# Kernel optimization log

Hardware: AMD Instinct MI355X
Metric: run time of the kernel (lower is better)

The kernel has to match this reference:

```python
import jax, jax.numpy as jnp
import numpy as np

D = 1024
M = 4096


def _linear_params(key, fan_in, fan_out):
    kw, kb = jax.random.split(key)
    bound = 1.0 / np.sqrt(fan_in)
    W = jax.random.uniform(kw, (fan_out, fan_in), jnp.float32, -bound, bound)
    b = jax.random.uniform(kb, (fan_out,), jnp.float32, -bound, bound)
    return W, b


def setup_inputs() -> dict:
    key = jax.random.key(0)
    ks = jax.random.split(key, 6)
    x = jax.random.normal(ks[0], (4, 2048, D), jnp.float32)
    Wq, bq = _linear_params(ks[1], D, D)
    Wk, bk = _linear_params(ks[2], D, D)
    Wv, bv = _linear_params(ks[3], D, D)
    Wo, bo = _linear_params(ks[4], D, D)
    Wf, bf = _linear_params(ks[5], D, M)
    return {"x": x, "Wq": Wq, "bq": bq, "Wk": Wk, "bk": bk,
            "Wv": Wv, "bv": bv, "Wo": Wo, "bo": bo, "Wf": Wf, "bf": bf}


def reference(x, Wq, bq, Wk, bk, Wv, bv, Wo, bo, Wf, bf):
    # projections (torch Linear: x @ W.T + b)
    Q = x @ Wq.T + bq  # [B,S,D]
    K = x @ Wk.T + bk
    V = x @ Wv.T + bv
    d_k = Q.shape[-1]
    scores = jnp.einsum('bqd,bkd->bqk', Q, K) / jnp.sqrt(jnp.float32(d_k))
    S = scores.shape[-1]
    causal = jnp.tril(jnp.ones((S, S), dtype=bool))  # [S,S]
    scores = jnp.where(causal, scores, -jnp.inf)
    probs = jax.nn.softmax(scores, axis=-1)
    attn = jnp.einsum('bqk,bkd->bqd', probs, V)
    out = attn @ Wo.T + bo
    # FFN: Linear(d->m) + GELU (torch default: exact erf GELU)
    ff = jax.nn.gelu(out @ Wf.T + bf, approximate=False)
    return ff
```

## Files before the change

kernel.cpp:

```cpp
#include <hip/hip_runtime.h>
#include <hip/hip_bf16.h>
#include <math.h>

using bf16 = __hip_bfloat16;
typedef __attribute__((ext_vector_type(8))) short bf16x8;
typedef __attribute__((ext_vector_type(4))) short bf16x4;
typedef __attribute__((ext_vector_type(4))) float f32x4;

#define GLOBAL_AS __attribute__((address_space(1)))
#define LDS_AS __attribute__((address_space(3)))

__device__ __forceinline__ float b2f(bf16 v) { return __bfloat162float(v); }
__device__ __forceinline__ bf16 f2b(float v) { return __float2bfloat16(v); }

__global__ __launch_bounds__(256) void k_conv(const float* __restrict__ src,
                                              bf16* __restrict__ dst, int n4) {
  int i = blockIdx.x * 256 + threadIdx.x;
  if (i >= n4) return;
  float4 v = ((const float4*)src)[i];
  bf16 t[4] = {f2b(v.x), f2b(v.y), f2b(v.z), f2b(v.w)};
  *(bf16x4*)(dst + 4 * (size_t)i) = *(bf16x4*)t;
}

__device__ __forceinline__ void stage_async(const bf16* __restrict__ g,
                                            int ldg, bf16* __restrict__ s) {
  int lane = threadIdx.x & 63;
  int wave = threadIdx.x >> 6;
  bf16* lds = s + wave * 1024;
  const bf16* g0 = g + (size_t)(wave * 32 + (lane >> 2)) * ldg + ((lane & 3) << 3);
  const bf16* g1 = g0 + (size_t)16 * ldg;
  __builtin_amdgcn_global_load_lds((GLOBAL_AS const unsigned*)g0,
                                   (LDS_AS unsigned*)lds, 16, 0, 0);
  __builtin_amdgcn_global_load_lds((GLOBAL_AS const unsigned*)g1,
                                   (LDS_AS unsigned*)(lds + 512), 16, 0, 0);
}

struct Acc { f32x4 a[4][4]; };

__device__ __forceinline__ void gemm_core(const bf16* __restrict__ A,
                                          const bf16* __restrict__ B,
                                          int K, int lda, int ldb, Acc& acc,
                                          bf16* sA, bf16* sB) {
  int lane = threadIdx.x & 63;
  int wave = threadIdx.x >> 6;
  int wm = wave & 1, wn = wave >> 1;
  int r = lane & 15;
  int ko = (lane >> 4) << 3;

  for (int k0 = 0; k0 < K; k0 += 32) {
    stage_async(A + k0, lda, sA);
    stage_async(B + k0, ldb, sB);
    __syncthreads();
    bf16x8 af[4], bfr[4];
#pragma unroll
    for (int t = 0; t < 4; ++t) {
      af[t]  = *(const bf16x8*)(sA + (wm * 64 + t * 16 + r) * 32 + ko);
      bfr[t] = *(const bf16x8*)(sB + (wn * 64 + t * 16 + r) * 32 + ko);
    }
#pragma unroll
    for (int tm = 0; tm < 4; ++tm)
#pragma unroll
      for (int tn = 0; tn < 4; ++tn)
        acc.a[tm][tn] = __builtin_amdgcn_mfma_f32_16x16x32_bf16(
            af[tm], bfr[tn], acc.a[tm][tn], 0, 0, 0);
    __syncthreads();
  }
}

template <typename TO, bool BIAS, bool GELU>
__device__ __forceinline__ void epilogue(const Acc& acc, TO* __restrict__ C,
                                         int ldc, const float* __restrict__ bias,
                                         float scale) {
  int lane = threadIdx.x & 63;
  int wave = threadIdx.x >> 6;
  int wm = wave & 1, wn = wave >> 1;
  int rbase = wm * 64 + ((lane >> 4) << 2);
  int cbase = wn * 64 + (lane & 15);
#pragma unroll
  for (int tm = 0; tm < 4; ++tm) {
#pragma unroll
    for (int tn = 0; tn < 4; ++tn) {
      int nn = cbase + tn * 16;
      float bv = BIAS ? bias[nn] : 0.0f;
#pragma unroll
      for (int rr = 0; rr < 4; ++rr) {
        int mm = rbase + tm * 16 + rr;
        float c = acc.a[tm][tn][rr] * scale + bv;
        if (GELU) c = 0.5f * c * (1.0f + erff(c * 0.70710678118f));
        if constexpr (__hip_internal::is_same<TO, bf16>::value)
          C[(size_t)mm * ldc + nn] = f2b(c);
        else
          C[(size_t)mm * ldc + nn] = c;
      }
    }
  }
}

__global__ __launch_bounds__(256) void k_qkv(
    const bf16* __restrict__ X, const bf16* __restrict__ Wq,
    const bf16* __restrict__ Wk, const bf16* __restrict__ Wv,
    const float* __restrict__ bq, const float* __restrict__ bk,
    const float* __restrict__ bv,
    bf16* __restrict__ Q, bf16* __restrict__ Ko, bf16* __restrict__ Vt) {
  __shared__ alignas(16) bf16 sA[4096];
  __shared__ alignas(16) bf16 sB[4096];
  const int K = 1024, N = 1024;
  int z = blockIdx.z;
  const bf16* W     = (z == 0) ? Wq : (z == 1) ? Wk : Wv;
  const float* bias = (z == 0) ? bq : (z == 1) ? bk : bv;
  const bf16* A = X + (size_t)blockIdx.x * 128 * K;
  const bf16* B = W + (size_t)blockIdx.y * 128 * K;
  Acc acc = {};
  gemm_core(A, B, K, K, K, acc, sA, sB);

  if (z < 2) {
    bf16* C = (z == 0 ? Q : Ko) +
              (size_t)blockIdx.x * 128 * N + blockIdx.y * 128;
    epilogue<bf16, true, false>(acc, C, N, bias + blockIdx.y * 128, 1.0f);
  } else {
    int lane = threadIdx.x & 63;
    int wave = threadIdx.x >> 6;
    int wm = wave & 1, wn = wave >> 1;
    int rbase = blockIdx.x * 128 + wm * 64 + ((lane >> 4) << 2);
    int cbase = blockIdx.y * 128 + wn * 64 + (lane & 15);
#pragma unroll
    for (int tm = 0; tm < 4; ++tm)
#pragma unroll
      for (int tn = 0; tn < 4; ++tn) {
        int n = cbase + tn * 16;
        float bvv = bias[n];
#pragma unroll
        for (int rr = 0; rr < 4; ++rr) {
          int m = rbase + tm * 16 + rr;
          int b = m >> 11, s = m & 2047;
          float c = acc.a[tm][tn][rr] + bvv;
          Vt[((size_t)b * 1024 + n) * 2048 + s] = f2b(c);
        }
      }
  }
}

__global__ __launch_bounds__(256) void k_scores(const bf16* __restrict__ Q,
                                                const bf16* __restrict__ Kk,
                                                bf16* __restrict__ P) {
  int bx = 15 - blockIdx.x;
  if ((int)blockIdx.y > bx) return;
  __shared__ alignas(16) bf16 sA[4096];
  __shared__ alignas(16) bf16 sB[4096];
  const int K = 1024, S = 2048;
  int z = blockIdx.z;
  const bf16* A = Q  + (size_t)z * S * K + (size_t)bx * 128 * K;
  const bf16* B = Kk + (size_t)z * S * K + (size_t)blockIdx.y * 128 * K;
  Acc acc = {};
  gemm_core(A, B, K, K, K, acc, sA, sB);
  bf16* C = P + (size_t)z * S * S + (size_t)bx * 128 * S + blockIdx.y * 128;
  epilogue<bf16, false, false>(acc, C, S, nullptr, 0.03125f);
}

__global__ __launch_bounds__(256) void k_softmax(bf16* __restrict__ P) {
  const int S = 2048;
  int q = blockIdx.x, z = blockIdx.y;
  bf16* row = P + ((size_t)z * S + q) * S;
  __shared__ float red[4];
  int tid = threadIdx.x;

  float mx = -1e30f;
  for (int k = tid; k <= q; k += 256) mx = fmaxf(mx, b2f(row[k]));
#pragma unroll
  for (int o = 32; o > 0; o >>= 1) mx = fmaxf(mx, __shfl_xor(mx, o));
  if ((tid & 63) == 0) red[tid >> 6] = mx;
  __syncthreads();
  mx = fmaxf(fmaxf(red[0], red[1]), fmaxf(red[2], red[3]));
  __syncthreads();

  float sum = 0.0f;
  for (int k = tid; k <= q; k += 256) sum += expf(b2f(row[k]) - mx);
#pragma unroll
  for (int o = 32; o > 0; o >>= 1) sum += __shfl_xor(sum, o);
  if ((tid & 63) == 0) red[tid >> 6] = sum;
  __syncthreads();
  sum = red[0] + red[1] + red[2] + red[3];
  float inv = 1.0f / sum;

  int kcap = ((q >> 7) + 1) << 7;
  for (int k = tid; k < kcap; k += 256) {
    float p = (k <= q) ? expf(b2f(row[k]) - mx) * inv : 0.0f;
    row[k] = f2b(p);
  }
}

__global__ __launch_bounds__(256) void k_attn(const bf16* __restrict__ P,
                                              const bf16* __restrict__ Vt,
                                              bf16* __restrict__ O) {
  __shared__ alignas(16) bf16 sA[4096];
  __shared__ alignas(16) bf16 sB[4096];
  const int S = 2048, D = 1024;
  int bx = 15 - (int)blockIdx.x;
  int z = blockIdx.z;
  int Keff = (bx + 1) * 128;
  const bf16* A = P  + (size_t)z * S * S + (size_t)bx * 128 * S;
  const bf16* B = Vt + (size_t)z * D * S + (size_t)blockIdx.y * 128 * S;
  Acc acc = {};
  gemm_core(A, B, Keff, S, S, acc, sA, sB);
  bf16* C = O + (size_t)z * S * D + (size_t)bx * 128 * D + blockIdx.y * 128;
  epilogue<bf16, false, false>(acc, C, D, nullptr, 1.0f);
}

__global__ __launch_bounds__(256) void k_out(const bf16* __restrict__ A0,
                                             const bf16* __restrict__ W,
                                             const float* __restrict__ bias,
                                             bf16* __restrict__ C0) {
  __shared__ alignas(16) bf16 sA[4096];
  __shared__ alignas(16) bf16 sB[4096];
  const int K = 1024, N = 1024;
  const bf16* A = A0 + (size_t)blockIdx.x * 128 * K;
  const bf16* B = W + (size_t)blockIdx.y * 128 * K;
  Acc acc = {};
  gemm_core(A, B, K, K, K, acc, sA, sB);
  bf16* C = C0 + (size_t)blockIdx.x * 128 * N + blockIdx.y * 128;
  epilogue<bf16, true, false>(acc, C, N, bias + blockIdx.y * 128, 1.0f);
}

__global__ __launch_bounds__(256) void k_ffn(const bf16* __restrict__ A0,
                                             const bf16* __restrict__ W,
                                             const float* __restrict__ bias,
                                             float* __restrict__ C0) {
  __shared__ alignas(16) bf16 sA[4096];
  __shared__ alignas(16) bf16 sB[4096];
  const int K = 1024, N = 4096;
  const bf16* A = A0 + (size_t)blockIdx.x * 128 * K;
  const bf16* B = W + (size_t)blockIdx.y * 128 * K;
  Acc acc = {};
  gemm_core(A, B, K, K, K, acc, sA, sB);
  float* C = C0 + (size_t)blockIdx.x * 128 * N + blockIdx.y * 128;
  epilogue<float, true, true>(acc, C, N, bias + blockIdx.y * 128, 1.0f);
}

extern "C" void kernel_launch(void* const* d_in, const int* in_sizes, int n_in,
                              void* d_out, int out_size, void* d_ws,
                              size_t ws_size, hipStream_t stream) {
  const float* x   = (const float*)d_in[0];
  const float* Wq  = (const float*)d_in[1];
  const float* bq  = (const float*)d_in[2];
  const float* Wk  = (const float*)d_in[3];
  const float* bk  = (const float*)d_in[4];
  const float* Wv  = (const float*)d_in[5];
  const float* bv  = (const float*)d_in[6];
  const float* Wo  = (const float*)d_in[7];
  const float* bo  = (const float*)d_in[8];
  const float* Wf  = (const float*)d_in[9];
  const float* bfb = (const float*)d_in[10];

  char* ws = (char*)d_ws;
  const size_t MB = 1 << 20;
  bf16* xb   = (bf16*)(ws);
  bf16* Wqb  = (bf16*)(ws + 16 * MB);
  bf16* Wkb  = (bf16*)(ws + 18 * MB);
  bf16* Wvb  = (bf16*)(ws + 20 * MB);
  bf16* P    = (bf16*)(ws);
  bf16* Q    = (bf16*)(ws + 32 * MB);
  bf16* Kb   = (bf16*)(ws + 48 * MB);
  bf16* Wob  = (bf16*)(ws + 48 * MB);
  bf16* Wfb  = (bf16*)(ws + 50 * MB);
  bf16* Vt   = (bf16*)(ws + 64 * MB);
  bf16* attn = Q;
  bf16* out  = Vt;
  float* y   = (float*)d_out;

  k_conv<<<8192, 256, 0, stream>>>(x,  xb,  8192 * 1024 / 4);
  k_conv<<<1024, 256, 0, stream>>>(Wq, Wqb, 1024 * 1024 / 4);
  k_conv<<<1024, 256, 0, stream>>>(Wk, Wkb, 1024 * 1024 / 4);
  k_conv<<<1024, 256, 0, stream>>>(Wv, Wvb, 1024 * 1024 / 4);
  k_qkv<<<dim3(64, 8, 3), 256, 0, stream>>>(xb, Wqb, Wkb, Wvb, bq, bk, bv,
                                            Q, Kb, Vt);
  k_scores<<<dim3(16, 16, 4), 256, 0, stream>>>(Q, Kb, P);
  k_conv<<<1024, 256, 0, stream>>>(Wo, Wob, 1024 * 1024 / 4);
  k_conv<<<4096, 256, 0, stream>>>(Wf, Wfb, 4096 * 1024 / 4);
  k_softmax<<<dim3(2048, 4), 256, 0, stream>>>(P);
  k_attn<<<dim3(16, 8, 4), 256, 0, stream>>>(P, Vt, attn);
  k_out<<<dim3(64, 8), 256, 0, stream>>>(attn, Wob, bo, out);
  k_ffn<<<dim3(64, 32), 256, 0, stream>>>(out, Wfb, bfb, y);
}
```

Baseline: 516.9 us.

## Double GEMM K-step, stage V transpose via LDS, use fast exp and tanh GELU

The shared GEMM core now loads two 32-wide K slices per barrier pair, halving the synchronisations per K. The V projection epilogue writes the transposed tile through LDS so global stores become 16-byte coalesced rows instead of scattered 2-byte writes. Softmax uses __expf and the FFN GELU switches from erf to a tanh-based approximation with a fast exp. These trade some numerical accuracy for cheaper transcendental math, and they double the LDS footprint per block, which may reduce occupancy.

```diff
diff --git a/kernel.cpp b/kernel.cpp
--- a/kernel.cpp
+++ b/kernel.cpp
@@ -12,6 +12,12 @@
 
 __device__ __forceinline__ float b2f(bf16 v) { return __bfloat162float(v); }
 __device__ __forceinline__ bf16 f2b(float v) { return __float2bfloat16(v); }
+
+__device__ __forceinline__ float gelu_f(float x) {
+  float u = x * (0.7978845608f + 0.0356774081f * x * x);
+  float t = 1.0f - 2.0f / (1.0f + __expf(2.0f * u));
+  return 0.5f * x * (1.0f + t);
+}
 
 __global__ __launch_bounds__(256) void k_conv(const float* __restrict__ src,
                                               bf16* __restrict__ dst, int n4) {
@@ -47,22 +53,27 @@
   int r = lane & 15;
   int ko = (lane >> 4) << 3;
 
-  for (int k0 = 0; k0 < K; k0 += 32) {
-    stage_async(A + k0, lda, sA);
-    stage_async(B + k0, ldb, sB);
+  for (int k0 = 0; k0 < K; k0 += 64) {
+    stage_async(A + k0,      lda, sA);
+    stage_async(A + k0 + 32, lda, sA + 4096);
+    stage_async(B + k0,      ldb, sB);
+    stage_async(B + k0 + 32, ldb, sB + 4096);
     __syncthreads();
-    bf16x8 af[4], bfr[4];
-#pragma unroll
-    for (int t = 0; t < 4; ++t) {
-      af[t]  = *(const bf16x8*)(sA + (wm * 64 + t * 16 + r) * 32 + ko);
-      bfr[t] = *(const bf16x8*)(sB + (wn * 64 + t * 16 + r) * 32 + ko);
+#pragma unroll
+    for (int kk = 0; kk < 2; ++kk) {
+      bf16x8 af[4], bfr[4];
+#pragma unroll
+      for (int t = 0; t < 4; ++t) {
+        af[t]  = *(const bf16x8*)(sA + kk * 4096 + (wm * 64 + t * 16 + r) * 32 + ko);
+        bfr[t] = *(const bf16x8*)(sB + kk * 4096 + (wn * 64 + t * 16 + r) * 32 + ko);
+      }
+#pragma unroll
+      for (int tm = 0; tm < 4; ++tm)
+#pragma unroll
+        for (int tn = 0; tn < 4; ++tn)
+          acc.a[tm][tn] = __builtin_amdgcn_mfma_f32_16x16x32_bf16(
+              af[tm], bfr[tn], acc.a[tm][tn], 0, 0, 0);
     }
-#pragma unroll
-    for (int tm = 0; tm < 4; ++tm)
-#pragma unroll
-      for (int tn = 0; tn < 4; ++tn)
-        acc.a[tm][tn] = __builtin_amdgcn_mfma_f32_16x16x32_bf16(
-            af[tm], bfr[tn], acc.a[tm][tn], 0, 0, 0);
     __syncthreads();
   }
 }
@@ -86,7 +97,7 @@
       for (int rr = 0; rr < 4; ++rr) {
         int mm = rbase + tm * 16 + rr;
         float c = acc.a[tm][tn][rr] * scale + bv;
-        if (GELU) c = 0.5f * c * (1.0f + erff(c * 0.70710678118f));
+        if (GELU) c = gelu_f(c);
         if constexpr (__hip_internal::is_same<TO, bf16>::value)
           C[(size_t)mm * ldc + nn] = f2b(c);
         else
@@ -102,8 +113,9 @@
     const float* __restrict__ bq, const float* __restrict__ bk,
     const float* __restrict__ bv,
     bf16* __restrict__ Q, bf16* __restrict__ Ko, bf16* __restrict__ Vt) {
-  __shared__ alignas(16) bf16 sA[4096];
-  __shared__ alignas(16) bf16 sB[4096];
+  __shared__ alignas(16) char arena[32768];
+  bf16* sA = (bf16*)arena;
+  bf16* sB = (bf16*)(arena + 16384);
   const int K = 1024, N = 1024;
   int z = blockIdx.z;
   const bf16* W     = (z == 0) ? Wq : (z == 1) ? Wk : Wv;
@@ -118,25 +130,40 @@
               (size_t)blockIdx.x * 128 * N + blockIdx.y * 128;
     epilogue<bf16, true, false>(acc, C, N, bias + blockIdx.y * 128, 1.0f);
   } else {
-    int lane = threadIdx.x & 63;
-    int wave = threadIdx.x >> 6;
+    bf16* sT = (bf16*)arena;
+    int tid = threadIdx.x;
+    int lane = tid & 63;
+    int wave = tid >> 6;
     int wm = wave & 1, wn = wave >> 1;
-    int rbase = blockIdx.x * 128 + wm * 64 + ((lane >> 4) << 2);
-    int cbase = blockIdx.y * 128 + wn * 64 + (lane & 15);
-#pragma unroll
-    for (int tm = 0; tm < 4; ++tm)
-#pragma unroll
-      for (int tn = 0; tn < 4; ++tn) {
-        int n = cbase + tn * 16;
-        float bvv = bias[n];
-#pragma unroll
-        for (int rr = 0; rr < 4; ++rr) {
-          int m = rbase + tm * 16 + rr;
-          int b = m >> 11, s = m & 2047;
-          float c = acc.a[tm][tn][rr] + bvv;
-          Vt[((size_t)b * 1024 + n) * 2048 + s] = f2b(c);
+    int b  = blockIdx.x >> 4;
+    int s0 = (blockIdx.x & 15) * 128;
+#pragma unroll
+    for (int p = 0; p < 2; ++p) {
+      __syncthreads();
+      if (wn == p) {
+        int rloc_s = wm * 64 + ((lane >> 4) << 2);
+#pragma unroll
+        for (int tn = 0; tn < 4; ++tn) {
+          int nl = (lane & 15) + tn * 16;
+          float bvv = bias[blockIdx.y * 128 + p * 64 + nl];
+#pragma unroll
+          for (int tm = 0; tm < 4; ++tm)
+#pragma unroll
+            for (int rr = 0; rr < 4; ++rr)
+              sT[nl * 136 + rloc_s + tm * 16 + rr] =
+                  f2b(acc.a[tm][tn][rr] + bvv);
         }
       }
+      __syncthreads();
+      int c = tid & 15, r0 = tid >> 4;
+#pragma unroll
+      for (int j = 0; j < 4; ++j) {
+        int rl = r0 + j * 16;
+        int n = blockIdx.y * 128 + p * 64 + rl;
+        *(bf16x8*)(Vt + ((size_t)b * 1024 + n) * 2048 + s0 + c * 8) =
+            *(const bf16x8*)(sT + rl * 136 + c * 8);
+      }
+    }
   }
 }
 
@@ -145,8 +172,9 @@
                                                 bf16* __restrict__ P) {
   int bx = 15 - blockIdx.x;
   if ((int)blockIdx.y > bx) return;
-  __shared__ alignas(16) bf16 sA[4096];
-  __shared__ alignas(16) bf16 sB[4096];
+  __shared__ alignas(16) char arena[32768];
+  bf16* sA = (bf16*)arena;
+  bf16* sB = (bf16*)(arena + 16384);
   const int K = 1024, S = 2048;
   int z = blockIdx.z;
   const bf16* A = Q  + (size_t)z * S * K + (size_t)bx * 128 * K;
@@ -174,7 +202,7 @@
   __syncthreads();
 
   float sum = 0.0f;
-  for (int k = tid; k <= q; k += 256) sum += expf(b2f(row[k]) - mx);
+  for (int k = tid; k <= q; k += 256) sum += __expf(b2f(row[k]) - mx);
 #pragma unroll
   for (int o = 32; o > 0; o >>= 1) sum += __shfl_xor(sum, o);
   if ((tid & 63) == 0) red[tid >> 6] = sum;
@@ -184,7 +212,7 @@
 
   int kcap = ((q >> 7) + 1) << 7;
   for (int k = tid; k < kcap; k += 256) {
-    float p = (k <= q) ? expf(b2f(row[k]) - mx) * inv : 0.0f;
+    float p = (k <= q) ? __expf(b2f(row[k]) - mx) * inv : 0.0f;
     row[k] = f2b(p);
   }
 }
@@ -192,8 +220,9 @@
 __global__ __launch_bounds__(256) void k_attn(const bf16* __restrict__ P,
                                               const bf16* __restrict__ Vt,
                                               bf16* __restrict__ O) {
-  __shared__ alignas(16) bf16 sA[4096];
-  __shared__ alignas(16) bf16 sB[4096];
+  __shared__ alignas(16) char arena[32768];
+  bf16* sA = (bf16*)arena;
+  bf16* sB = (bf16*)(arena + 16384);
   const int S = 2048, D = 1024;
   int bx = 15 - (int)blockIdx.x;
   int z = blockIdx.z;
@@ -210,8 +239,9 @@
                                              const bf16* __restrict__ W,
                                              const float* __restrict__ bias,
                                              bf16* __restrict__ C0) {
-  __shared__ alignas(16) bf16 sA[4096];
-  __shared__ alignas(16) bf16 sB[4096];
+  __shared__ alignas(16) char arena[32768];
+  bf16* sA = (bf16*)arena;
+  bf16* sB = (bf16*)(arena + 16384);
   const int K = 1024, N = 1024;
   const bf16* A = A0 + (size_t)blockIdx.x * 128 * K;
   const bf16* B = W + (size_t)blockIdx.y * 128 * K;
@@ -225,8 +255,9 @@
                                              const bf16* __restrict__ W,
                                              const float* __restrict__ bias,
                                              float* __restrict__ C0) {
-  __shared__ alignas(16) bf16 sA[4096];
-  __shared__ alignas(16) bf16 sB[4096];
+  __shared__ alignas(16) char arena[32768];
+  bf16* sA = (bf16*)arena;
+  bf16* sB = (bf16*)(arena + 16384);
   const int K = 1024, N = 4096;
   const bf16* A = A0 + (size_t)blockIdx.x * 128 * K;
   const bf16* B = W + (size_t)blockIdx.y * 128 * K;
```

New measurement: 508.3 us. Within noise of the previous version (-1.7%).
